# Kernel tuning notes

Hardware: AMD Instinct MI355X
Metric: run time of the kernel (lower is better)

Reference implementation:

```python
import jax, jax.numpy as jnp
import numpy as np

B, L, D_ENC = 32, 512, 512
STEPS = 32
E_DIM = 128      # embedding_dim
A_DIM = 256      # attention_dim
H = 512          # hidden_size
VOCAB = 32000


def _linear(x, W, b):
    return x @ W.T + b


def setup_inputs() -> dict:
    key = jax.random.key(0)
    ks = jax.random.split(key, 12)
    s = lambda fan_in: 1.0 / np.sqrt(fan_in)
    return {
        "encoder_outputs": jax.random.normal(ks[0], (B, L, D_ENC), dtype=jnp.float32),
        "target_seq": jax.random.randint(ks[1], (B, STEPS), 0, VOCAB, dtype=jnp.int64),
        "pos_embedding": jax.random.normal(ks[2], (STEPS, E_DIM), dtype=jnp.float32),
        "dec_proj_W": jax.random.uniform(ks[3], (A_DIM, E_DIM), minval=-s(E_DIM), maxval=s(E_DIM)),
        "dec_proj_b": jnp.zeros((A_DIM,), jnp.float32),
        "enc_proj_W": jax.random.uniform(ks[4], (A_DIM, D_ENC), minval=-s(D_ENC), maxval=s(D_ENC)),
        "enc_proj_b": jnp.zeros((A_DIM,), jnp.float32),
        "attn_score_W": jax.random.uniform(ks[5], (1, A_DIM), minval=-s(A_DIM), maxval=s(A_DIM)),
        "attn_score_b": jnp.zeros((1,), jnp.float32),
        "hidden_proj_W": jax.random.uniform(ks[6], (H, E_DIM), minval=-s(E_DIM), maxval=s(E_DIM)),
        "hidden_proj_b": jnp.zeros((H,), jnp.float32),
        "fc_out_W": jax.random.uniform(ks[7], (VOCAB, H + D_ENC), minval=-s(H + D_ENC), maxval=s(H + D_ENC)),
        "fc_out_b": jnp.zeros((VOCAB,), jnp.float32),
    }


def reference(encoder_outputs, target_seq, pos_embedding,
              dec_proj_W, dec_proj_b, enc_proj_W, enc_proj_b,
              attn_score_W, attn_score_b, hidden_proj_W, hidden_proj_b,
              fc_out_W, fc_out_b):
    batch = encoder_outputs.shape[0]
    steps = target_seq.shape[1]
    # [B, L, A]
    enc_proj = _linear(encoder_outputs, enc_proj_W, enc_proj_b)
    # [B, S, E]  (dropout=0 in eval)
    pos_emb = jnp.broadcast_to(pos_embedding[:steps][None], (batch, steps, pos_embedding.shape[1]))
    # [B, S, A]
    dec_query = _linear(pos_emb, dec_proj_W, dec_proj_b)
    # additive attention: [B, S, L, A]
    combined = jnp.tanh(enc_proj[:, None, :, :] + dec_query[:, :, None, :])
    # score reduction to scalar: [B, S, L]
    attn_scores = jnp.einsum('bsla,a->bsl', combined, attn_score_W[0]) + attn_score_b[0]
    attn_weights = jax.nn.softmax(attn_scores, axis=2)
    # context: [B, S, D_enc]
    context = jnp.einsum('bsl,bld->bsd', attn_weights, encoder_outputs)
    hidden = _linear(pos_emb, hidden_proj_W, hidden_proj_b)  # [B, S, H]
    logits = _linear(jnp.concatenate([hidden, context], axis=-1), fc_out_W, fc_out_b)
    return logits
```

## Files before the change

kernel.cpp:

```cpp
#include <hip/hip_runtime.h>
#include <hip/hip_bf16.h>
#include <stdint.h>

typedef __attribute__((ext_vector_type(4))) float f32x4;
typedef __attribute__((ext_vector_type(8))) short short8;

#define B_   32
#define L_   512
#define DE_  512
#define S_   32
#define ED_  128
#define AD_  256
#define HD_  512
#define VOC_ 32000
#define M_   1024

__device__ __forceinline__ unsigned short f2bf(float f){
  union { float f; unsigned int u; } v; v.f = f;
  unsigned int u = v.u;
  unsigned int r = (u + 0x7FFFu + ((u >> 16) & 1u)) >> 16;
  return (unsigned short)r;
}

__device__ __forceinline__ float bf2f(unsigned short u){
  union { unsigned int u; float f; } v; v.u = ((unsigned int)u) << 16;
  return v.f;
}

__device__ __forceinline__ float tanh_fast(float x){
  float t = __expf(2.0f * x);
  return (t - 1.0f) * __builtin_amdgcn_rcpf(t + 1.0f);
}

__device__ __forceinline__ void gl_lds16(const void* g, void* l){
  __builtin_amdgcn_global_load_lds(
      (const __attribute__((address_space(1))) unsigned int*)g,
      (__attribute__((address_space(3))) unsigned int*)l, 16, 0, 0);
}

extern "C" __global__ void __launch_bounds__(256)
k_prep(const float* __restrict__ enc, unsigned short* __restrict__ enc_bf,
       const float* __restrict__ eW, unsigned short* __restrict__ encW_bf,
       const float* __restrict__ pos,
       const float* __restrict__ dW, const float* __restrict__ db,
       const float* __restrict__ hW, const float* __restrict__ hb,
       float* __restrict__ dq, unsigned short* __restrict__ hbf){
  int blk = blockIdx.x, tid = threadIdx.x;
  if (blk < 8192){
    int i = blk * 256 + tid;
    f32x4 v = ((const f32x4*)enc)[i];
    ushort4 o;
    o.x = f2bf(v[0]); o.y = f2bf(v[1]); o.z = f2bf(v[2]); o.w = f2bf(v[3]);
    ((ushort4*)enc_bf)[i] = o;
  } else if (blk < 8320){
    int i = (blk - 8192) * 256 + tid;
    f32x4 v = ((const f32x4*)eW)[i];
    ushort4 o;
    o.x = f2bf(v[0]); o.y = f2bf(v[1]); o.z = f2bf(v[2]); o.w = f2bf(v[3]);
    ((ushort4*)encW_bf)[i] = o;
  } else {
    int t = (blk - 8320) * 256 + tid;
    if (t < S_ * AD_){
      int s = t >> 8, a = t & 255;
      const float* p = pos + s * ED_;
      const float* wrow = dW + a * ED_;
      float acc = db[a];
      #pragma unroll 4
      for (int e = 0; e < ED_; ++e) acc += p[e] * wrow[e];
      dq[t] = acc;
    } else if (t < S_ * AD_ + S_ * HD_){
      int u = t - S_ * AD_;
      int s = u >> 9, h = u & 511;
      const float* p = pos + s * ED_;
      const float* wrow = hW + h * ED_;
      float acc = hb[h];
      #pragma unroll 4
      for (int e = 0; e < ED_; ++e) acc += p[e] * wrow[e];
      hbf[u] = f2bf(acc);
    }
  }
}

extern "C" __global__ void __launch_bounds__(256, 4)
k_gemm_encp(const unsigned short* __restrict__ A, const unsigned short* __restrict__ Bt,
            const float* __restrict__ bias, unsigned short* __restrict__ C){
  __shared__ unsigned short As[2][128 * 32];
  __shared__ unsigned short Bs[2][128 * 32];
  int bm = blockIdx.x >> 1, bn = blockIdx.x & 1;
  int tid = threadIdx.x, wid = tid >> 6, lane = tid & 63;
  int fr = lane & 15, fq = lane >> 4;
  int wm = wid >> 1, wn = wid & 1;
  int srow = lane >> 2;
  int scol = ((lane & 3) ^ ((lane >> 3) & 3)) * 8;
  int c0 = wid * 2;
  const unsigned short* aS0 = A  + (size_t)(bm * 128 + c0 * 16 + srow) * 512 + scol;
  const unsigned short* aS1 = aS0 + (size_t)16 * 512;
  const unsigned short* bS0 = Bt + (size_t)(bn * 128 + c0 * 16 + srow) * 512 + scol;
  const unsigned short* bS1 = bS0 + (size_t)16 * 512;
  int swzfq = (fq ^ ((fr >> 1) & 3)) * 8;

  f32x4 acc[4][4];
  #pragma unroll
  for (int i = 0; i < 4; ++i)
    #pragma unroll
    for (int j = 0; j < 4; ++j) acc[i][j] = (f32x4)0.0f;

#define STAGE_E(buf, kk) do { \
    gl_lds16(aS0 + (kk), &As[buf][c0 * 512]); \
    gl_lds16(aS1 + (kk), &As[buf][c0 * 512 + 512]); \
    gl_lds16(bS0 + (kk), &Bs[buf][c0 * 512]); \
    gl_lds16(bS1 + (kk), &Bs[buf][c0 * 512 + 512]); \
  } while (0)

  STAGE_E(0, 0);
  __syncthreads();

  int cur = 0;
  for (int t = 0; t < 16; ++t){
    if (t < 15) STAGE_E(cur ^ 1, (size_t)(t + 1) * 32);
    short8 a[4], b[4];
    #pragma unroll
    for (int mf = 0; mf < 4; ++mf) a[mf] = *(const short8*)&As[cur][(wm * 64 + mf * 16 + fr) * 32 + swzfq];
    #pragma unroll
    for (int nf = 0; nf < 4; ++nf) b[nf] = *(const short8*)&Bs[cur][(wn * 64 + nf * 16 + fr) * 32 + swzfq];
    #pragma unroll
    for (int mf = 0; mf < 4; ++mf)
      #pragma unroll
      for (int nf = 0; nf < 4; ++nf)
        acc[mf][nf] = __builtin_amdgcn_mfma_f32_16x16x32_bf16(a[mf], b[nf], acc[mf][nf], 0, 0, 0);
    __syncthreads();
    cur ^= 1;
  }
#undef STAGE_E

  #pragma unroll
  for (int mf = 0; mf < 4; ++mf){
    int row = bm * 128 + wm * 64 + mf * 16 + fq * 4;
    #pragma unroll
    for (int nf = 0; nf < 4; ++nf){
      int col = bn * 128 + wn * 64 + nf * 16 + fr;
      float bv = bias[col];
      #pragma unroll
      for (int j = 0; j < 4; ++j)
        C[(size_t)(row + j) * 256 + col] = f2bf(acc[mf][nf][j] + bv);
    }
  }
}

extern "C" __global__ void __launch_bounds__(256)
k_mid(const float* __restrict__ fcW, const unsigned short* __restrict__ hbf,
      const float* __restrict__ fcb, unsigned short* __restrict__ Wc,
      float* __restrict__ logh,
      const unsigned short* __restrict__ encp, const float* __restrict__ dq,
      const float* __restrict__ vW, float* __restrict__ scoreT){
  __shared__ char smem[49152];
  int blk = blockIdx.x;
  if (blk < 500){
    int bn = blk;
    int tid = threadIdx.x, wid = tid >> 6, lane = tid & 63;
    int fr = lane & 15, fq = lane >> 4;
    #pragma unroll 8
    for (int i = 0; i < 32; ++i){
      int idx = i * 256 + tid;
      int row = idx >> 7, c4 = idx & 127;
      f32x4 v = *(const f32x4*)&fcW[(size_t)(bn * 64 + row) * 1024 + 512 + c4 * 4];
      ushort4 o;
      o.x = f2bf(v[0]); o.y = f2bf(v[1]); o.z = f2bf(v[2]); o.w = f2bf(v[3]);
      *(ushort4*)&Wc[(size_t)(bn * 64 + row) * 512 + c4 * 4] = o;
    }
    int col = bn * 64 + wid * 16 + fr;
    const float* brow = fcW + (size_t)col * 1024;
    f32x4 acc0 = (f32x4)0.0f, acc1 = (f32x4)0.0f;
    #pragma unroll 4
    for (int k0 = 0; k0 < 512; k0 += 32){
      int ko = k0 + fq * 8;
      f32x4 b0 = *(const f32x4*)(brow + ko);
      f32x4 b1 = *(const f32x4*)(brow + ko + 4);
      short8 bfr;
      bfr[0] = (short)f2bf(b0[0]); bfr[1] = (short)f2bf(b0[1]);
      bfr[2] = (short)f2bf(b0[2]); bfr[3] = (short)f2bf(b0[3]);
      bfr[4] = (short)f2bf(b1[0]); bfr[5] = (short)f2bf(b1[1]);
      bfr[6] = (short)f2bf(b1[2]); bfr[7] = (short)f2bf(b1[3]);
      short8 a0 = *(const short8*)&hbf[(size_t)fr * 512 + ko];
      short8 a1 = *(const short8*)&hbf[(size_t)(16 + fr) * 512 + ko];
      acc0 = __builtin_amdgcn_mfma_f32_16x16x32_bf16(a0, bfr, acc0, 0, 0, 0);
      acc1 = __builtin_amdgcn_mfma_f32_16x16x32_bf16(a1, bfr, acc1, 0, 0, 0);
    }
    float bv = fcb[col];
    #pragma unroll
    for (int j = 0; j < 4; ++j){
      logh[(size_t)(fq * 4 + j) * VOC_ + col]      = acc0[j] + bv;
      logh[(size_t)(16 + fq * 4 + j) * VOC_ + col] = acc1[j] + bv;
    }
  } else {
    unsigned short* eL = (unsigned short*)smem;
    float* pp = (float*)(smem + 16384);
    int blk2 = blk - 500;
    int b = blk2 >> 4, c = blk2 & 15;
    int tid = threadIdx.x, w = tid >> 6, lane = tid & 63;
    #pragma unroll
    for (int i = 0; i < 4; ++i){
      int rb = i * 8 + w * 2;
      gl_lds16(encp + (size_t)(b * 512 + c * 32 + rb + (lane >> 5)) * 256 + (lane & 31) * 8,
               &eL[rb * 256]);
    }
    int s = tid >> 3, g = tid & 7;
    f32x4 dqv[8], vv[8];
    #pragma unroll
    for (int k = 0; k < 8; ++k){
      dqv[k] = *(const f32x4*)&dq[s * 256 + g * 32 + k * 4];
      vv[k]  = *(const f32x4*)&vW[g * 32 + k * 4];
    }
    __syncthreads();
    #pragma unroll 4
    for (int l = 0; l < 32; ++l){
      float a = 0.0f;
      #pragma unroll
      for (int k = 0; k < 8; ++k){
        uint2 e4 = *(const uint2*)&eL[l * 256 + g * 32 + k * 4];
        a += tanh_fast(bf2f((unsigned short)(e4.x & 0xffff)) + dqv[k][0]) * vv[k][0];
        a += tanh_fast(bf2f((unsigned short)(e4.x >> 16))    + dqv[k][1]) * vv[k][1];
        a += tanh_fast(bf2f((unsigned short)(e4.y & 0xffff)) + dqv[k][2]) * vv[k][2];
        a += tanh_fast(bf2f((unsigned short)(e4.y >> 16))    + dqv[k][3]) * vv[k][3];
      }
      pp[l * 256 + tid] = a;
    }
    __syncthreads();
    #pragma unroll
    for (int k2 = 0; k2 < 4; ++k2){
      int p = tid + k2 * 256;
      int l = p >> 5, ss = p & 31;
      f32x4 x0 = *(const f32x4*)&pp[p * 8];
      f32x4 x1 = *(const f32x4*)&pp[p * 8 + 4];
      float sum = (x0[0] + x0[1]) + (x0[2] + x0[3]) + ((x1[0] + x1[1]) + (x1[2] + x1[3]));
      scoreT[((size_t)b * 512 + c * 32 + l) * 32 + ss] = sum;
    }
  }
}

extern "C" __global__ void __launch_bounds__(256)
k_smax(const float* __restrict__ scoreT, float* __restrict__ wgt){
  __shared__ float sL[512 * 32];
  __shared__ float pm[32][8], ps[32][8];
  __shared__ float Mf[32], invf[32];
  int b = blockIdx.x, tid = threadIdx.x;
  for (int idx = tid; idx < 16384; idx += 256){
    int l = idx >> 5, s2 = idx & 31;
    sL[l * 32 + (s2 ^ (l & 31))] = scoreT[(size_t)b * 16384 + idx];
  }
  __syncthreads();
  int s2 = tid & 31, part = tid >> 5;
  float m = -1e30f;
  for (int l = part * 64; l < part * 64 + 64; ++l)
    m = fmaxf(m, sL[l * 32 + (s2 ^ (l & 31))]);
  pm[s2][part] = m;
  __syncthreads();
  float M = pm[s2][0];
  #pragma unroll
  for (int j2 = 1; j2 < 8; ++j2) M = fmaxf(M, pm[s2][j2]);
  float sum = 0.0f;
  for (int l = part * 64; l < part * 64 + 64; ++l)
    sum += __expf(sL[l * 32 + (s2 ^ (l & 31))] - M);
  ps[s2][part] = sum;
  __syncthreads();
  if (part == 0){
    float L = ps[s2][0];
    #pragma unroll
    for (int j2 = 1; j2 < 8; ++j2) L += ps[s2][j2];
    Mf[s2] = M;
    invf[s2] = __builtin_amdgcn_rcpf(L);
  }
  __syncthreads();
  for (int idx = tid; idx < 16384; idx += 256){
    int ss = idx >> 9, l = idx & 511;
    float x = sL[l * 32 + (ss ^ (l & 31))];
    wgt[(size_t)(b * 32 + ss) * 512 + l] = __expf(x - Mf[ss]) * invf[ss];
  }
}

extern "C" __global__ void __launch_bounds__(256)
k_ctx(const unsigned short* __restrict__ encb, const float* __restrict__ wgt,
      unsigned short* __restrict__ ctx){
  int b = blockIdx.x >> 4, dt = blockIdx.x & 15;
  int tid = threadIdx.x;
  __shared__ float wl[32 * 512];
  #pragma unroll 8
  for (int i = 0; i < 64; ++i)
    wl[i * 256 + tid] = wgt[(size_t)b * 16384 + i * 256 + tid];
  __syncthreads();
  int d = dt * 32 + (tid & 31);
  int grp = tid >> 5;
  float acc0 = 0, acc1 = 0, acc2 = 0, acc3 = 0;
  const unsigned short* ebase = encb + (size_t)b * 262144 + d;
  const float* w0 = &wl[(grp * 4 + 0) * 512];
  const float* w1 = &wl[(grp * 4 + 1) * 512];
  const float* w2 = &wl[(grp * 4 + 2) * 512];
  const float* w3 = &wl[(grp * 4 + 3) * 512];
  #pragma unroll 8
  for (int l = 0; l < 512; ++l){
    float e = bf2f(ebase[(size_t)l * 512]);
    acc0 += w0[l] * e; acc1 += w1[l] * e; acc2 += w2[l] * e; acc3 += w3[l] * e;
  }
  size_t obase = (size_t)(b * 32 + grp * 4) * 512 + d;
  ctx[obase]        = f2bf(acc0);
  ctx[obase + 512]  = f2bf(acc1);
  ctx[obase + 1024] = f2bf(acc2);
  ctx[obase + 1536] = f2bf(acc3);
}

extern "C" __global__ void __launch_bounds__(512, 4)
k_gemm_main(const unsigned short* __restrict__ Abf, const unsigned short* __restrict__ Wc,
            const float* __restrict__ logh, float* __restrict__ out){
  __shared__ unsigned short As[2][128 * 32];
  __shared__ unsigned short Bs[3][256 * 32];
  int orig = blockIdx.x;
  int wg = (orig & 7) * 125 + (orig >> 3);
  int bm = wg & 7, bn = wg >> 3;
  int tid = threadIdx.x, wid = tid >> 6, lane = tid & 63;
  int fr = lane & 15, fq = lane >> 4;
  int wm = wid >> 2, wn = wid & 3;
  int abase = bm * 128, bbase = bn * 256;
  int srow = lane >> 2;
  int scol = ((lane & 3) ^ ((lane >> 3) & 3)) * 8;
  const unsigned short* aS0 = Abf + (size_t)(abase + wid * 16 + srow) * 512 + scol;
  const unsigned short* bS0 = Wc  + (size_t)(bbase + wid * 32 + srow) * 512 + scol;
  const unsigned short* bS1 = bS0 + (size_t)16 * 512;
  int swzfq = (fq ^ ((fr >> 1) & 3)) * 8;

  f32x4 acc[4][4];
  #pragma unroll
  for (int i = 0; i < 4; ++i)
    #pragma unroll
    for (int jj = 0; jj < 4; ++jj) acc[i][jj] = (f32x4)0.0f;

#define STAGE_A(buf, kk) gl_lds16(aS0 + (kk), &As[buf][wid * 512])
#define STAGE_B(buf, kk) do { \
    gl_lds16(bS0 + (kk), &Bs[buf][wid * 1024]); \
    gl_lds16(bS1 + (kk), &Bs[buf][wid * 1024 + 512]); \
  } while (0)

  STAGE_A(0, 0);
  STAGE_B(0, 0);
  STAGE_B(1, 32);
  asm volatile("s_waitcnt vmcnt(2)" ::: "memory");
  __builtin_amdgcn_s_barrier();
  __builtin_amdgcn_sched_barrier(0);

  #pragma unroll
  for (int t = 0; t < 16; ++t){
    const int ca = t & 1, cb = t % 3;
    short8 a[4], b[4];
    if (t < 15) STAGE_A(ca ^ 1, (size_t)(t + 1) * 32);
    #pragma unroll
    for (int nf = 0; nf < 4; ++nf)
      b[nf] = *(const short8*)&Bs[cb][(wn * 64 + nf * 16 + fr) * 32 + swzfq];
    #pragma unroll
    for (int mf = 0; mf < 2; ++mf)
      a[mf] = *(const short8*)&As[ca][(wm * 64 + mf * 16 + fr) * 32 + swzfq];
    __builtin_amdgcn_s_setprio(1);
    #pragma unroll
    for (int mf = 0; mf < 2; ++mf)
      #pragma unroll
      for (int nf = 0; nf < 4; ++nf)
        acc[mf][nf] = __builtin_amdgcn_mfma_f32_16x16x32_bf16(a[mf], b[nf], acc[mf][nf], 0, 0, 0);
    __builtin_amdgcn_s_setprio(0);
    if (t < 14) STAGE_B((t + 2) % 3, (size_t)(t + 2) * 32);
    #pragma unroll
    for (int mf = 2; mf < 4; ++mf)
      a[mf] = *(const short8*)&As[ca][(wm * 64 + mf * 16 + fr) * 32 + swzfq];
    __builtin_amdgcn_s_setprio(1);
    #pragma unroll
    for (int mf = 2; mf < 4; ++mf)
      #pragma unroll
      for (int nf = 0; nf < 4; ++nf)
        acc[mf][nf] = __builtin_amdgcn_mfma_f32_16x16x32_bf16(a[mf], b[nf], acc[mf][nf], 0, 0, 0);
    __builtin_amdgcn_s_setprio(0);
    if (t < 14)       asm volatile("s_waitcnt vmcnt(2)" ::: "memory");
    else if (t == 14) asm volatile("s_waitcnt vmcnt(0)" ::: "memory");
    if (t < 15){
      __builtin_amdgcn_s_barrier();
      __builtin_amdgcn_sched_barrier(0);
    }
  }
#undef STAGE_A
#undef STAGE_B

  #pragma unroll
  for (int mf = 0; mf < 4; ++mf){
    int rowb = bm * 128 + wm * 64 + mf * 16 + fq * 4;
    #pragma unroll
    for (int nf = 0; nf < 4; ++nf){
      int col = bn * 256 + wn * 64 + nf * 16 + fr;
      #pragma unroll
      for (int jj = 0; jj < 4; ++jj){
        int r = rowb + jj;
        out[(size_t)r * VOC_ + col] = acc[mf][nf][jj] + logh[(size_t)(r & 31) * VOC_ + col];
      }
    }
  }
}

extern "C" void kernel_launch(void* const* d_in, const int* in_sizes, int n_in,
                              void* d_out, int out_size, void* d_ws, size_t ws_size,
                              hipStream_t stream){
  const float* enc = (const float*)d_in[0];
  const float* pos = (const float*)d_in[2];
  const float* dW  = (const float*)d_in[3];
  const float* db  = (const float*)d_in[4];
  const float* eW  = (const float*)d_in[5];
  const float* eb  = (const float*)d_in[6];
  const float* vW  = (const float*)d_in[7];
  const float* hW  = (const float*)d_in[9];
  const float* hb  = (const float*)d_in[10];
  const float* fcW = (const float*)d_in[11];
  const float* fcb = (const float*)d_in[12];
  float* out = (float*)d_out;

  char* w = (char*)d_ws;
  unsigned short* Wc_bf   = (unsigned short*)(w);
  unsigned short* enc_bf  = (unsigned short*)(w + 32768000);
  unsigned short* encp_bf = (unsigned short*)(w + 49545216);
  unsigned short* ctx     = (unsigned short*)(w + 57933824);
  float*          logh    = (float*)(w + 58982400);
  float*          dq      = (float*)(w + 63078400);
  unsigned short* hbf     = (unsigned short*)(w + 63111168);
  unsigned short* encW_bf = (unsigned short*)(w + 63143936);
  float*          wgt     = (float*)(w + 63406080);
  float*          scoreT  = (float*)(w + 65503232);

  k_prep<<<dim3(8416), dim3(256), 0, stream>>>(enc, enc_bf, eW, encW_bf,
                                               pos, dW, db, hW, hb, dq, hbf);
  k_gemm_encp<<<dim3(256), dim3(256), 0, stream>>>(enc_bf, encW_bf, eb, encp_bf);
  k_mid<<<dim3(1012), dim3(256), 0, stream>>>(fcW, hbf, fcb, Wc_bf, logh,
                                              encp_bf, dq, vW, scoreT);
  k_smax<<<dim3(32), dim3(256), 0, stream>>>(scoreT, wgt);
  k_ctx<<<dim3(512), dim3(256), 0, stream>>>(enc_bf, wgt, ctx);
  k_gemm_main<<<dim3(1000), dim3(512), 0, stream>>>(ctx, Wc_bf, logh, out);
}
```

Baseline: 218.0 us.

## Fuse softmax into context kernel and simplify tanh via pre-scaled exp2

Several separate changes. The softmax kernel is merged into the context kernel, so each context block recomputes softmax for its batch from the raw scores in LDS, which drops one launch and the weight buffer round trip. The tanh scoring is rewritten as V - 2*sum(v/(exp2(x)+1)), with the 2*log2(e) factor folded into the enc projection and dq outputs, which saves per-element work. The score blocks are halved to 16 rows each, doubling the block count for better occupancy, and LDS is accessed with swizzles to avoid bank conflicts. The cost is 16x redundant softmax computation across the dt blocks, and enc_proj is now stored in bf16 after scaling.

```diff
diff --git a/kernel.cpp b/kernel.cpp
--- a/kernel.cpp
+++ b/kernel.cpp
@@ -14,6 +14,7 @@
 #define HD_  512
 #define VOC_ 32000
 #define M_   1024
+#define SCL_ 2.885390081777927f
 
 __device__ __forceinline__ unsigned short f2bf(float f){
   union { float f; unsigned int u; } v; v.f = f;
@@ -25,11 +26,6 @@
 __device__ __forceinline__ float bf2f(unsigned short u){
   union { unsigned int u; float f; } v; v.u = ((unsigned int)u) << 16;
   return v.f;
-}
-
-__device__ __forceinline__ float tanh_fast(float x){
-  float t = __expf(2.0f * x);
-  return (t - 1.0f) * __builtin_amdgcn_rcpf(t + 1.0f);
 }
 
 __device__ __forceinline__ void gl_lds16(const void* g, void* l){
@@ -67,7 +63,7 @@
       float acc = db[a];
       #pragma unroll 4
       for (int e = 0; e < ED_; ++e) acc += p[e] * wrow[e];
-      dq[t] = acc;
+      dq[t] = SCL_ * acc;
     } else if (t < S_ * AD_ + S_ * HD_){
       int u = t - S_ * AD_;
       int s = u >> 9, h = u & 511;
@@ -142,7 +138,7 @@
       float bv = bias[col];
       #pragma unroll
       for (int j = 0; j < 4; ++j)
-        C[(size_t)(row + j) * 256 + col] = f2bf(acc[mf][nf][j] + bv);
+        C[(size_t)(row + j) * 256 + col] = f2bf(SCL_ * (acc[mf][nf][j] + bv));
     }
   }
 }
@@ -153,7 +149,7 @@
       float* __restrict__ logh,
       const unsigned short* __restrict__ encp, const float* __restrict__ dq,
       const float* __restrict__ vW, float* __restrict__ scoreT){
-  __shared__ char smem[49152];
+  __shared__ char smem[24576];
   int blk = blockIdx.x;
   if (blk < 500){
     int bn = blk;
@@ -194,15 +190,19 @@
     }
   } else {
     unsigned short* eL = (unsigned short*)smem;
-    float* pp = (float*)(smem + 16384);
+    float* pp = (float*)(smem + 8192);
     int blk2 = blk - 500;
-    int b = blk2 >> 4, c = blk2 & 15;
+    int b = blk2 >> 5, c = blk2 & 31;
     int tid = threadIdx.x, w = tid >> 6, lane = tid & 63;
-    #pragma unroll
-    for (int i = 0; i < 4; ++i){
-      int rb = i * 8 + w * 2;
-      gl_lds16(encp + (size_t)(b * 512 + c * 32 + rb + (lane >> 5)) * 256 + (lane & 31) * 8,
-               &eL[rb * 256]);
+    {
+      int sl = lane & 31;
+      int srcgrp = (sl & 7) * 4 + (sl >> 3);
+      #pragma unroll
+      for (int i = 0; i < 2; ++i){
+        int rb = i * 8 + w * 2;
+        gl_lds16(encp + (size_t)(b * 512 + c * 16 + rb + (lane >> 5)) * 256 + srcgrp * 8,
+                 &eL[rb * 256]);
+      }
     }
     int s = tid >> 3, g = tid & 7;
     f32x4 dqv[8], vv[8];
@@ -211,97 +211,101 @@
       dqv[k] = *(const f32x4*)&dq[s * 256 + g * 32 + k * 4];
       vv[k]  = *(const f32x4*)&vW[g * 32 + k * 4];
     }
+    float Vg = 0.0f;
+    #pragma unroll
+    for (int k = 0; k < 8; ++k)
+      Vg += (vv[k][0] + vv[k][1]) + (vv[k][2] + vv[k][3]);
     __syncthreads();
-    #pragma unroll 4
-    for (int l = 0; l < 32; ++l){
-      float a = 0.0f;
-      #pragma unroll
-      for (int k = 0; k < 8; ++k){
-        uint2 e4 = *(const uint2*)&eL[l * 256 + g * 32 + k * 4];
-        a += tanh_fast(bf2f((unsigned short)(e4.x & 0xffff)) + dqv[k][0]) * vv[k][0];
-        a += tanh_fast(bf2f((unsigned short)(e4.x >> 16))    + dqv[k][1]) * vv[k][1];
-        a += tanh_fast(bf2f((unsigned short)(e4.y & 0xffff)) + dqv[k][2]) * vv[k][2];
-        a += tanh_fast(bf2f((unsigned short)(e4.y >> 16))    + dqv[k][3]) * vv[k][3];
+    #pragma unroll 2
+    for (int l = 0; l < 16; ++l){
+      float acc = 0.0f;
+      #pragma unroll
+      for (int k2 = 0; k2 < 4; ++k2){
+        short8 e8 = *(const short8*)&eL[l * 256 + (g + k2 * 8) * 8];
+        const unsigned int* u = (const unsigned int*)&e8;
+        #pragma unroll
+        for (int j = 0; j < 2; ++j){
+          int k = k2 * 2 + j;
+          unsigned int w0 = u[j * 2], w1 = u[j * 2 + 1];
+          float t0 = exp2f(__uint_as_float(w0 << 16)          + dqv[k][0]);
+          float t1 = exp2f(__uint_as_float(w0 & 0xffff0000u)  + dqv[k][1]);
+          float t2 = exp2f(__uint_as_float(w1 << 16)          + dqv[k][2]);
+          float t3 = exp2f(__uint_as_float(w1 & 0xffff0000u)  + dqv[k][3]);
+          acc = fmaf(vv[k][0], __builtin_amdgcn_rcpf(t0 + 1.0f), acc);
+          acc = fmaf(vv[k][1], __builtin_amdgcn_rcpf(t1 + 1.0f), acc);
+          acc = fmaf(vv[k][2], __builtin_amdgcn_rcpf(t2 + 1.0f), acc);
+          acc = fmaf(vv[k][3], __builtin_amdgcn_rcpf(t3 + 1.0f), acc);
+        }
       }
-      pp[l * 256 + tid] = a;
+      pp[l * 256 + tid] = fmaf(-2.0f, acc, Vg);
     }
     __syncthreads();
     #pragma unroll
-    for (int k2 = 0; k2 < 4; ++k2){
-      int p = tid + k2 * 256;
+    for (int kk = 0; kk < 2; ++kk){
+      int p = tid + kk * 256;
       int l = p >> 5, ss = p & 31;
       f32x4 x0 = *(const f32x4*)&pp[p * 8];
       f32x4 x1 = *(const f32x4*)&pp[p * 8 + 4];
       float sum = (x0[0] + x0[1]) + (x0[2] + x0[3]) + ((x1[0] + x1[1]) + (x1[2] + x1[3]));
-      scoreT[((size_t)b * 512 + c * 32 + l) * 32 + ss] = sum;
+      scoreT[((size_t)b * 512 + c * 16 + l) * 32 + ss] = sum;
     }
   }
 }
 
 extern "C" __global__ void __launch_bounds__(256)
-k_smax(const float* __restrict__ scoreT, float* __restrict__ wgt){
-  __shared__ float sL[512 * 32];
+k_ctx(const unsigned short* __restrict__ encb, const float* __restrict__ scoreT,
+      unsigned short* __restrict__ ctx){
+  __shared__ float wl[32 * 512];
   __shared__ float pm[32][8], ps[32][8];
   __shared__ float Mf[32], invf[32];
-  int b = blockIdx.x, tid = threadIdx.x;
+  int b = blockIdx.x >> 4, dt = blockIdx.x & 15;
+  int tid = threadIdx.x;
   for (int idx = tid; idx < 16384; idx += 256){
-    int l = idx >> 5, s2 = idx & 31;
-    sL[l * 32 + (s2 ^ (l & 31))] = scoreT[(size_t)b * 16384 + idx];
+    int l = idx >> 5, s = idx & 31;
+    wl[s * 512 + (l ^ s)] = scoreT[(size_t)b * 16384 + idx];
   }
   __syncthreads();
   int s2 = tid & 31, part = tid >> 5;
   float m = -1e30f;
   for (int l = part * 64; l < part * 64 + 64; ++l)
-    m = fmaxf(m, sL[l * 32 + (s2 ^ (l & 31))]);
+    m = fmaxf(m, wl[s2 * 512 + (l ^ s2)]);
   pm[s2][part] = m;
   __syncthreads();
   float M = pm[s2][0];
   #pragma unroll
-  for (int j2 = 1; j2 < 8; ++j2) M = fmaxf(M, pm[s2][j2]);
+  for (int j = 1; j < 8; ++j) M = fmaxf(M, pm[s2][j]);
   float sum = 0.0f;
   for (int l = part * 64; l < part * 64 + 64; ++l)
-    sum += __expf(sL[l * 32 + (s2 ^ (l & 31))] - M);
+    sum += __expf(wl[s2 * 512 + (l ^ s2)] - M);
   ps[s2][part] = sum;
   __syncthreads();
   if (part == 0){
-    float L = ps[s2][0];
-    #pragma unroll
-    for (int j2 = 1; j2 < 8; ++j2) L += ps[s2][j2];
+    float Lt = ps[s2][0];
+    #pragma unroll
+    for (int j = 1; j < 8; ++j) Lt += ps[s2][j];
     Mf[s2] = M;
-    invf[s2] = __builtin_amdgcn_rcpf(L);
-  }
-  __syncthreads();
-  for (int idx = tid; idx < 16384; idx += 256){
-    int ss = idx >> 9, l = idx & 511;
-    float x = sL[l * 32 + (ss ^ (l & 31))];
-    wgt[(size_t)(b * 32 + ss) * 512 + l] = __expf(x - Mf[ss]) * invf[ss];
-  }
-}
-
-extern "C" __global__ void __launch_bounds__(256)
-k_ctx(const unsigned short* __restrict__ encb, const float* __restrict__ wgt,
-      unsigned short* __restrict__ ctx){
-  int b = blockIdx.x >> 4, dt = blockIdx.x & 15;
-  int tid = threadIdx.x;
-  __shared__ float wl[32 * 512];
-  #pragma unroll 8
-  for (int i = 0; i < 64; ++i)
-    wl[i * 256 + tid] = wgt[(size_t)b * 16384 + i * 256 + tid];
+    invf[s2] = __builtin_amdgcn_rcpf(Lt);
+  }
+  __syncthreads();
+  for (int l = part * 64; l < part * 64 + 64; ++l){
+    int a = s2 * 512 + (l ^ s2);
+    wl[a] = __expf(wl[a] - Mf[s2]) * invf[s2];
+  }
   __syncthreads();
   int d = dt * 32 + (tid & 31);
   int grp = tid >> 5;
+  int r0 = grp * 4, r1 = r0 + 1, r2 = r0 + 2, r3 = r0 + 3;
   float acc0 = 0, acc1 = 0, acc2 = 0, acc3 = 0;
   const unsigned short* ebase = encb + (size_t)b * 262144 + d;
-  const float* w0 = &wl[(grp * 4 + 0) * 512];
-  const float* w1 = &wl[(grp * 4 + 1) * 512];
-  const float* w2 = &wl[(grp * 4 + 2) * 512];
-  const float* w3 = &wl[(grp * 4 + 3) * 512];
   #pragma unroll 8
   for (int l = 0; l < 512; ++l){
     float e = bf2f(ebase[(size_t)l * 512]);
-    acc0 += w0[l] * e; acc1 += w1[l] * e; acc2 += w2[l] * e; acc3 += w3[l] * e;
-  }
-  size_t obase = (size_t)(b * 32 + grp * 4) * 512 + d;
+    acc0 = fmaf(wl[r0 * 512 + (l ^ r0)], e, acc0);
+    acc1 = fmaf(wl[r1 * 512 + (l ^ r1)], e, acc1);
+    acc2 = fmaf(wl[r2 * 512 + (l ^ r2)], e, acc2);
+    acc3 = fmaf(wl[r3 * 512 + (l ^ r3)], e, acc3);
+  }
+  size_t obase = (size_t)(b * 32 + r0) * 512 + d;
   ctx[obase]        = f2bf(acc0);
   ctx[obase + 512]  = f2bf(acc1);
   ctx[obase + 1024] = f2bf(acc2);
@@ -425,15 +429,13 @@
   float*          dq      = (float*)(w + 63078400);
   unsigned short* hbf     = (unsigned short*)(w + 63111168);
   unsigned short* encW_bf = (unsigned short*)(w + 63143936);
-  float*          wgt     = (float*)(w + 63406080);
-  float*          scoreT  = (float*)(w + 65503232);
+  float*          scoreT  = (float*)(w + 63406080);
 
   k_prep<<<dim3(8416), dim3(256), 0, stream>>>(enc, enc_bf, eW, encW_bf,
                                                pos, dW, db, hW, hb, dq, hbf);
   k_gemm_encp<<<dim3(256), dim3(256), 0, stream>>>(enc_bf, encW_bf, eb, encp_bf);
-  k_mid<<<dim3(1012), dim3(256), 0, stream>>>(fcW, hbf, fcb, Wc_bf, logh,
+  k_mid<<<dim3(1524), dim3(256), 0, stream>>>(fcW, hbf, fcb, Wc_bf, logh,
                                               encp_bf, dq, vW, scoreT);
-  k_smax<<<dim3(32), dim3(256), 0, stream>>>(scoreT, wgt);
-  k_ctx<<<dim3(512), dim3(256), 0, stream>>>(enc_bf, wgt, ctx);
+  k_ctx<<<dim3(512), dim3(256), 0, stream>>>(enc_bf, scoreT, ctx);
   k_gemm_main<<<dim3(1000), dim3(512), 0, stream>>>(ctx, Wc_bf, logh, out);
 }
```

After: 215.1 us. Within noise of the previous version (-1.3%).
